# Optimization experiments

Hardware: AMD Instinct MI355X
Metric: run time of the kernel (lower is better)

## Reference

```python
import jax, jax.numpy as jnp
import numpy as np

WS = 8
HEADS = 12


def _dwconv(x, w, b):
    # x: (N, C, H, W); w: (C, 1, 3, 3) depthwise, zero pad 1
    y = jax.lax.conv_general_dilated(
        x, w, window_strides=(1, 1), padding=((1, 1), (1, 1)),
        dimension_numbers=("NCHW", "OIHW", "NCHW"), feature_group_count=x.shape[1])
    return y + b[None, :, None, None]


def _sepconv(x, dw, db, pw, pb):
    y = _dwconv(x, dw, db)
    # pointwise 1x1 conv: (N,C,H,W) x (O,C) -> (N,O,H,W)
    return jnp.einsum("nchw,oc->nohw", y, pw) + pb[None, :, None, None]


def _rel_pos_index(ws):
    coords = np.stack(np.meshgrid(np.arange(ws), np.arange(ws), indexing="ij"))  # (2, ws, ws)
    cf = coords.reshape(2, -1)
    rel = cf[:, :, None] - cf[:, None, :]          # (2, ws*ws, ws*ws)
    rel = rel.transpose(1, 2, 0).copy()
    rel[..., 0] += ws - 1
    rel[..., 1] += ws - 1
    rel[..., 0] *= 2 * ws - 1
    return rel.sum(-1)                             # (ws*ws, ws*ws)


def setup_inputs() -> dict:
    key = jax.random.key(0)
    ks = jax.random.split(key, 16)
    B, T, C, H, W = 2, 1, 384, 192, 192
    s = 0.02
    inp = {
        "vid": jax.random.normal(ks[0], (B, T, C, H, W), jnp.float32),
        "qd_w": jax.random.normal(ks[1], (C, 1, 3, 3), jnp.float32) * s,
        "qd_b": jnp.zeros((C,), jnp.float32),
        "qp_w": jax.random.normal(ks[2], (C, C), jnp.float32) * s,
        "qp_b": jnp.zeros((C,), jnp.float32),
        "kd_w": jax.random.normal(ks[3], (C, 1, 3, 3), jnp.float32) * s,
        "kd_b": jnp.zeros((C,), jnp.float32),
        "kp_w": jax.random.normal(ks[4], (C, C), jnp.float32) * s,
        "kp_b": jnp.zeros((C,), jnp.float32),
        "vd_w": jax.random.normal(ks[5], (C, 1, 3, 3), jnp.float32) * s,
        "vd_b": jnp.zeros((C,), jnp.float32),
        "vp_w": jax.random.normal(ks[6], (C, C), jnp.float32) * s,
        "vp_b": jnp.zeros((C,), jnp.float32),
        "rpb_table": jax.random.normal(ks[7], ((2 * WS - 1) ** 2, HEADS), jnp.float32) * s,
        "proj_w": jax.random.normal(ks[8], (C, C), jnp.float32) * s,
        "proj_b": jnp.zeros((C,), jnp.float32),
    }
    return inp


def reference(vid, qd_w, qd_b, qp_w, qp_b, kd_w, kd_b, kp_w, kp_b,
              vd_w, vd_b, vp_w, vp_b, rpb_table, proj_w, proj_b):
    B, T, C, H, W = vid.shape
    heads, ws = HEADS, WS
    hd = C // heads
    scale = hd ** -0.5
    x = vid.reshape(B * T, C, H, W)

    q = _sepconv(x, qd_w, qd_b, qp_w, qp_b) * scale
    k = _sepconv(x, kd_w, kd_b, kp_w, kp_b)
    v = _sepconv(x, vd_w, vd_b, vp_w, vp_b)

    nh, nw = H // ws, W // ws

    def win(z):  # (N, C, H, W) -> (N*nh*nw, heads, ws*ws, hd)
        N = z.shape[0]
        z = z.reshape(N, heads, hd, nh, ws, nw, ws)
        z = z.transpose(0, 3, 5, 1, 4, 6, 2)  # N, nh, nw, heads, ws, ws, hd
        return z.reshape(N * nh * nw, heads, ws * ws, hd)

    qw, kw, vw = win(q), win(k), win(v)

    # product search within window (dists = q . k), rel-pos bias softmax
    attn = jnp.einsum("nhqd,nhkd->nhqk", qw, kw)
    rp_idx = _rel_pos_index(ws)  # static (64, 64)
    bias = rpb_table[rp_idx.reshape(-1)].reshape(ws * ws, ws * ws, heads)
    bias = bias.transpose(2, 0, 1)  # (heads, 64, 64)
    attn = jax.nn.softmax(attn + bias[None], axis=-1)

    # weighted patch sum (ps=1 -> pixels)
    out = jnp.einsum("nhqk,nhkd->nhqd", attn, vw)  # (N*nh*nw, heads, ws*ws, hd)

    # un-window, merge heads into (h c) channel order, then token projection
    out = out.reshape(B * T, nh, nw, heads, ws, ws, hd)
    out = out.transpose(0, 1, 4, 2, 5, 3, 6).reshape(B * T, H, W, heads * hd)
    out = out @ proj_w.T + proj_b

    # fold (ps=1, stride0=1): identity overlap-add, zvid == 1
    out = out.transpose(0, 3, 1, 2).reshape(B, T, C, H, W)
    return out
```

## Files before the change

### kernel.cpp

```cpp
#include <hip/hip_runtime.h>

#define CCH 384
#define HH 192
#define WWD 192
#define NIMG 2
#define HWP (HH * WWD)
#define PTOT (NIMG * HWP)
#define HEADS 12
#define HD 32
#define NWIN 24
#define WINS 576
#define EELEM ((size_t)NIMG * CCH * HWP)
#define WMAT 147456

typedef __attribute__((ext_vector_type(8))) short bh8;
typedef __attribute__((ext_vector_type(8))) unsigned short us8;
typedef __attribute__((ext_vector_type(4))) unsigned short us4;
typedef __attribute__((ext_vector_type(4))) float fx4;

__device__ __forceinline__ unsigned short f2bf(float f) {
    unsigned u = __float_as_uint(f);
    u += 0x7fffu + ((u >> 16) & 1u);
    return (unsigned short)(u >> 16);
}

__device__ __forceinline__ void gload16(const void* g, void* l) {
    __builtin_amdgcn_global_load_lds(
        (const __attribute__((address_space(1))) void*)g,
        (__attribute__((address_space(3))) void*)l, 16, 0, 0);
}

__global__ __launch_bounds__(256) void prep(
    const float* __restrict__ qp, const float* __restrict__ kp,
    const float* __restrict__ vp, const float* __restrict__ pj,
    const float* __restrict__ qd, const float* __restrict__ kd,
    const float* __restrict__ vd, const float* __restrict__ rpb,
    unsigned short* __restrict__ Wb, float* __restrict__ dwT,
    float* __restrict__ Bx)
{
    int bx = blockIdx.x;
    if (bx < 288) {
        int idx8 = (bx * 256 + threadIdx.x) * 8;
        int which = idx8 / WMAT;
        int loc = idx8 - which * WMAT;
        const float* s = (which == 0) ? qp : (which == 1) ? kp : (which == 2) ? vp : pj;
        float4 v0 = *(const float4*)(s + loc);
        float4 v1 = *(const float4*)(s + loc + 4);
        us8 ov;
        ov[0] = f2bf(v0.x); ov[1] = f2bf(v0.y); ov[2] = f2bf(v0.z); ov[3] = f2bf(v0.w);
        ov[4] = f2bf(v1.x); ov[5] = f2bf(v1.y); ov[6] = f2bf(v1.z); ov[7] = f2bf(v1.w);
        *(us8*)(Wb + idx8) = ov;
    } else if (bx < 329) {
        int idx = (bx - 288) * 256 + threadIdx.x;
        if (idx < 3 * 9 * CCH) {
            int ten = idx / (9 * CCH);
            int rem = idx - ten * (9 * CCH);
            int tap = rem / CCH;
            int c   = rem - tap * CCH;
            const float* s = (ten == 0) ? qd : (ten == 1) ? kd : vd;
            dwT[idx] = s[c * 9 + tap];
        }
    } else {
        int idx = (bx - 329) * 256 + threadIdx.x;
        int h  = idx >> 12;
        int tk = (idx >> 6) & 63;
        int tq = idx & 63;
        int dy = (tq >> 3) - (tk >> 3) + 7;
        int dx = (tq & 7) - (tk & 7) + 7;
        Bx[idx] = rpb[(dy * 15 + dx) * HEADS + h];
    }
}

__global__ __launch_bounds__(256) void dwgather(
    const float* __restrict__ x,
    const float* __restrict__ wt,
    const float* __restrict__ qb, const float* __restrict__ kb,
    const float* __restrict__ vb,
    unsigned short* __restrict__ oq, unsigned short* __restrict__ ok,
    unsigned short* __restrict__ ov)
{
    __shared__ float halo[64 * 121];

    int bid = blockIdx.x;
    int b = (bid & 7) * 864 + (bid >> 3);
    int wtx  = b % 24;
    int strip = b / 24;
    int chv  = strip % 6;
    int nwy  = strip / 6;
    int wy   = nwy % 24;
    int n    = nwy / 24;

    int h0 = wy * 8, w0 = wtx * 8;
    int tid = threadIdx.x;
    int c   = tid & 63;
    int pxg = tid >> 6;
    int cg  = chv * 64 + c;
    int widx = n * WINS + wy * NWIN + wtx;

    const float* xbase = x + (size_t)n * CCH * HWP + (size_t)(chv * 64) * HWP;

    for (int j = tid; j < 1920; j += 256) {
        int seg = j % 3;
        int t   = j / 3;
        int rr  = t % 10;
        int cc  = t / 10;
        int hr  = h0 - 1 + rr;
        int cb  = w0 - 2 + seg * 4;
        float4 val = make_float4(0.f, 0.f, 0.f, 0.f);
        if (hr >= 0 && hr < HH) {
            const float* p = xbase + (size_t)cc * HWP + (size_t)hr * WWD;
            if (cb >= 0 && cb + 4 <= WWD) {
                val = *(const float4*)(p + cb);
            } else {
                if (cb + 0 >= 0 && cb + 0 < WWD) val.x = p[cb + 0];
                if (cb + 1 >= 0 && cb + 1 < WWD) val.y = p[cb + 1];
                if (cb + 2 >= 0 && cb + 2 < WWD) val.z = p[cb + 2];
                if (cb + 3 >= 0 && cb + 3 < WWD) val.w = p[cb + 3];
            }
        }
        int hb = cc * 121 + rr * 12 + seg * 4;
        halo[hb + 0] = val.x;
        halo[hb + 1] = val.y;
        halo[hb + 2] = val.z;
        halo[hb + 3] = val.w;
    }

    float wq[9], wk[9], wv[9];
#pragma unroll
    for (int t = 0; t < 9; ++t) {
        wq[t] = wt[t * CCH + cg];
        wk[t] = wt[9 * CCH + t * CCH + cg];
        wv[t] = wt[18 * CCH + t * CCH + cg];
    }
    float bqv = qb[cg], bkv = kb[cg], bvv = vb[cg];

    __syncthreads();

    const int hbase = c * 121 + (2 * pxg) * 12;
    float r0[10], r1[10], r2[10];
#pragma unroll
    for (int cc = 0; cc < 10; ++cc) r0[cc] = halo[hbase + cc + 1];
#pragma unroll
    for (int cc = 0; cc < 10; ++cc) r1[cc] = halo[hbase + 12 + cc + 1];
#pragma unroll
    for (int cc = 0; cc < 10; ++cc) r2[cc] = halo[hbase + 24 + cc + 1];

    size_t ob0 = ((size_t)widx * 64 + pxg * 16) * CCH + cg;

#pragma unroll
    for (int pc = 0; pc < 8; ++pc) {
        float sq = 0.f, sk = 0.f, sv = 0.f;
#pragma unroll
        for (int dc = 0; dc < 3; ++dc) {
            float x0 = r0[pc + dc], x1 = r1[pc + dc], x2 = r2[pc + dc];
            sq = fmaf(x0, wq[dc], sq);     sk = fmaf(x0, wk[dc], sk);     sv = fmaf(x0, wv[dc], sv);
            sq = fmaf(x1, wq[3 + dc], sq); sk = fmaf(x1, wk[3 + dc], sk); sv = fmaf(x1, wv[3 + dc], sv);
            sq = fmaf(x2, wq[6 + dc], sq); sk = fmaf(x2, wk[6 + dc], sk); sv = fmaf(x2, wv[6 + dc], sv);
        }
        size_t o = ob0 + (size_t)pc * CCH;
        oq[o] = f2bf(sq + bqv);
        ok[o] = f2bf(sk + bkv);
        ov[o] = f2bf(sv + bvv);
    }

#pragma unroll
    for (int cc = 0; cc < 10; ++cc) r0[cc] = halo[hbase + 36 + cc + 1];

#pragma unroll
    for (int pc = 0; pc < 8; ++pc) {
        float sq = 0.f, sk = 0.f, sv = 0.f;
#pragma unroll
        for (int dc = 0; dc < 3; ++dc) {
            float x0 = r1[pc + dc], x1 = r2[pc + dc], x2 = r0[pc + dc];
            sq = fmaf(x0, wq[dc], sq);     sk = fmaf(x0, wk[dc], sk);     sv = fmaf(x0, wv[dc], sv);
            sq = fmaf(x1, wq[3 + dc], sq); sk = fmaf(x1, wk[3 + dc], sk); sv = fmaf(x1, wv[3 + dc], sv);
            sq = fmaf(x2, wq[6 + dc], sq); sk = fmaf(x2, wk[6 + dc], sk); sv = fmaf(x2, wv[6 + dc], sv);
        }
        size_t o = ob0 + (size_t)(8 + pc) * CCH;
        oq[o] = f2bf(sq + bqv);
        ok[o] = f2bf(sk + bkv);
        ov[o] = f2bf(sv + bvv);
    }
}

__global__ __launch_bounds__(256) void qkv_gemm(
    const unsigned short* __restrict__ tr0, const unsigned short* __restrict__ tr1,
    const unsigned short* __restrict__ tr2, const unsigned short* __restrict__ Wball,
    const float* __restrict__ qpb, const float* __restrict__ kpb,
    const float* __restrict__ vpb, float scale,
    unsigned short* __restrict__ qo, unsigned short* __restrict__ ko,
    unsigned short* __restrict__ vo)
{
    __shared__ __align__(16) char smem[33792];
    typedef unsigned short (*tile3)[128][32];
    tile3 Wt = (tile3)smem;
    tile3 Yt = (tile3)(smem + 16384);
    typedef unsigned short (*tep_t)[132];
    tep_t T16 = (tep_t)smem;

    int bL = blockIdx.x;
    int O  = (bL & 7) * 648 + (bL >> 3);
    int z  = O / 1728;
    int rem = O - z * 1728;
    int py = rem / 3;
    int cx = rem - py * 3;
    int pp0 = py * 128, cm0 = cx * 128;

    const unsigned short* Y  = (z == 0) ? tr0 : (z == 1) ? tr1 : tr2;
    const unsigned short* Wb = Wball + (size_t)z * WMAT;
    const float* bias        = (z == 0) ? qpb : (z == 1) ? kpb : vpb;
    float sc                 = (z == 0) ? scale : 1.0f;
    unsigned short* outb     = (z == 0) ? qo : (z == 1) ? ko : vo;
    bool vmode = (z == 2);

    int tid = threadIdx.x;
    int lid = tid & 63, wid = tid >> 6;
    int wr = wid >> 1, wc = wid & 1;
    int li = lid & 15, g = lid >> 4;

    int srow = (lid >> 2);
    int scol = (((lid & 3) ^ ((srow >> 1) & 3))) * 8;
    int gsw = (g ^ ((li >> 1) & 3)) * 8;

    fx4 acc[4][4];
#pragma unroll
    for (int i = 0; i < 4; ++i)
#pragma unroll
        for (int j = 0; j < 4; ++j) acc[i][j] = (fx4){0.f, 0.f, 0.f, 0.f};

    tile3 A3 = vmode ? Yt : Wt;
    tile3 B3 = vmode ? Wt : Yt;

    const unsigned short* Wg0 = Wb + (size_t)(cm0 + wid * 32 + srow) * CCH + scol;
    const unsigned short* Yg0 = Y  + (size_t)(pp0 + wid * 32 + srow) * CCH + scol;

#pragma unroll
    for (int qi = 0; qi < 2; ++qi) {
        gload16(Wg0 + (size_t)qi * 16 * CCH, &Wt[0][wid * 32 + qi * 16][0]);
        gload16(Yg0 + (size_t)qi * 16 * CCH, &Yt[0][wid * 32 + qi * 16][0]);
    }
    __syncthreads();

    for (int kt = 0; kt < 12; ++kt) {
        int cur = kt & 1;
        if (kt < 11) {
            int k1 = (kt + 1) * 32;
#pragma unroll
            for (int qi = 0; qi < 2; ++qi) {
                gload16(Wg0 + (size_t)qi * 16 * CCH + k1, &Wt[cur ^ 1][wid * 32 + qi * 16][0]);
                gload16(Yg0 + (size_t)qi * 16 * CCH + k1, &Yt[cur ^ 1][wid * 32 + qi * 16][0]);
            }
        }

        bh8 a[4], b[4];
#pragma unroll
        for (int mf = 0; mf < 4; ++mf)
            a[mf] = *(const bh8*)&A3[cur][wr * 64 + mf * 16 + li][gsw];
#pragma unroll
        for (int nf = 0; nf < 4; ++nf)
            b[nf] = *(const bh8*)&B3[cur][wc * 64 + nf * 16 + li][gsw];
#pragma unroll
        for (int mf = 0; mf < 4; ++mf)
#pragma unroll
            for (int nf = 0; nf < 4; ++nf)
                acc[mf][nf] = __builtin_amdgcn_mfma_f32_16x16x32_bf16(
                    a[mf], b[nf], acc[mf][nf], 0, 0, 0);

        __syncthreads();
    }

    if (!vmode) {
#pragma unroll
        for (int mf = 0; mf < 4; ++mf) {
            int cl = wr * 64 + mf * 16 + g * 4;
            float4 bv = *(const float4*)&bias[cm0 + cl];
#pragma unroll
            for (int nf = 0; nf < 4; ++nf) {
                int pl = wc * 64 + nf * 16 + li;
                us4 o;
                o[0] = f2bf((acc[mf][nf][0] + bv.x) * sc);
                o[1] = f2bf((acc[mf][nf][1] + bv.y) * sc);
                o[2] = f2bf((acc[mf][nf][2] + bv.z) * sc);
                o[3] = f2bf((acc[mf][nf][3] + bv.w) * sc);
                *(us4*)&T16[pl][cl] = o;
            }
        }
        __syncthreads();
#pragma unroll
        for (int it = 0; it < 8; ++it) {
            int row = it * 16 + wid * 4 + (lid >> 4);
            int col = (lid & 15) * 8;
            us8 vv = *(const us8*)&T16[row][col];
            *(us8*)(outb + (size_t)(pp0 + row) * CCH + cm0 + col) = vv;
        }
    } else {
#pragma unroll
        for (int nf = 0; nf < 4; ++nf) {
            int cl = wc * 64 + nf * 16 + li;
            float bv = bias[cm0 + cl];
#pragma unroll
            for (int mf = 0; mf < 4; ++mf) {
                int pl = wr * 64 + mf * 16 + g * 4;
                us4 o;
                o[0] = f2bf(acc[mf][nf][0] + bv);
                o[1] = f2bf(acc[mf][nf][1] + bv);
                o[2] = f2bf(acc[mf][nf][2] + bv);
                o[3] = f2bf(acc[mf][nf][3] + bv);
                *(us4*)&T16[cl][pl] = o;
            }
        }
        __syncthreads();
        int n = pp0 / HWP;
        int pl0 = pp0 - n * HWP;
#pragma unroll
        for (int it = 0; it < 8; ++it) {
            int row = it * 16 + wid * 4 + (lid >> 4);
            int col = (lid & 15) * 8;
            us8 vv = *(const us8*)&T16[row][col];
            *(us8*)(outb + (size_t)(n * CCH + cm0 + row) * HWP + pl0 + col) = vv;
        }
    }
}

__global__ __launch_bounds__(256) void proj_gemm(
    const unsigned short* __restrict__ Y, const unsigned short* __restrict__ Wb,
    const float* __restrict__ bias, float* __restrict__ outf)
{
    __shared__ unsigned short Wt[2][128][32];
    __shared__ unsigned short Yt[2][128][32];

    int bL = blockIdx.x;
    int O  = (bL & 7) * 216 + (bL >> 3);
    int py = O / 3;
    int cx = O - py * 3;
    int pp0 = py * 128, cm0 = cx * 128;

    int tid = threadIdx.x;
    int lid = tid & 63, wid = tid >> 6;
    int wr = wid >> 1, wc = wid & 1;
    int li = lid & 15, g = lid >> 4;

    int srow = (lid >> 2);
    int scol = (((lid & 3) ^ ((srow >> 1) & 3))) * 8;
    int gsw = (g ^ ((li >> 1) & 3)) * 8;

    fx4 acc[4][4];
#pragma unroll
    for (int i = 0; i < 4; ++i)
#pragma unroll
        for (int j = 0; j < 4; ++j) acc[i][j] = (fx4){0.f, 0.f, 0.f, 0.f};

    const unsigned short* Wg0 = Wb + (size_t)(cm0 + wid * 32 + srow) * CCH + scol;
    const unsigned short* Yg0 = Y  + (size_t)(pp0 + wid * 32 + srow) * CCH + scol;

#pragma unroll
    for (int qi = 0; qi < 2; ++qi) {
        gload16(Wg0 + (size_t)qi * 16 * CCH, &Wt[0][wid * 32 + qi * 16][0]);
        gload16(Yg0 + (size_t)qi * 16 * CCH, &Yt[0][wid * 32 + qi * 16][0]);
    }
    __syncthreads();

    for (int kt = 0; kt < 12; ++kt) {
        int cur = kt & 1;
        if (kt < 11) {
            int k1 = (kt + 1) * 32;
#pragma unroll
            for (int qi = 0; qi < 2; ++qi) {
                gload16(Wg0 + (size_t)qi * 16 * CCH + k1, &Wt[cur ^ 1][wid * 32 + qi * 16][0]);
                gload16(Yg0 + (size_t)qi * 16 * CCH + k1, &Yt[cur ^ 1][wid * 32 + qi * 16][0]);
            }
        }

        bh8 a[4], b[4];
#pragma unroll
        for (int mf = 0; mf < 4; ++mf)
            a[mf] = *(const bh8*)&Wt[cur][wr * 64 + mf * 16 + li][gsw];
#pragma unroll
        for (int nf = 0; nf < 4; ++nf)
            b[nf] = *(const bh8*)&Yt[cur][wc * 64 + nf * 16 + li][gsw];
#pragma unroll
        for (int mf = 0; mf < 4; ++mf)
#pragma unroll
            for (int nf = 0; nf < 4; ++nf)
                acc[mf][nf] = __builtin_amdgcn_mfma_f32_16x16x32_bf16(
                    a[mf], b[nf], acc[mf][nf], 0, 0, 0);

        __syncthreads();
    }

#pragma unroll
    for (int mf = 0; mf < 4; ++mf) {
        int c = cm0 + wr * 64 + mf * 16 + g * 4;
#pragma unroll
        for (int nf = 0; nf < 4; ++nf) {
            int p = pp0 + wc * 64 + nf * 16 + li;
            int n = p / HWP;
            int rem = p - n * HWP;
            int win = rem >> 6, t = rem & 63;
            int h = (win / NWIN) * 8 + (t >> 3);
            int w = (win % NWIN) * 8 + (t & 7);
            float* op = outf + (size_t)n * CCH * HWP + (size_t)h * WWD + w;
#pragma unroll
            for (int r = 0; r < 4; ++r)
                op[(size_t)(c + r) * HWP] = acc[mf][nf][r] + bias[c + r];
        }
    }
}

__global__ __launch_bounds__(256) void attn(
    const unsigned short* __restrict__ q, const unsigned short* __restrict__ k,
    const unsigned short* __restrict__ v, const float* __restrict__ Bx,
    unsigned short* __restrict__ o)
{
    __shared__ unsigned short Pl[4][64][72];

    int tid = threadIdx.x, lid = tid & 63, wid = tid >> 6;
    int wl = blockIdx.x;
    int n = wl / WINS, winl = wl - n * WINS;
    int li = lid & 15, g = lid >> 4;

    const fx4 z = (fx4){0.f, 0.f, 0.f, 0.f};

    for (int hq = wid; hq < HEADS; hq += 4) {
        const unsigned short* qp = q + (size_t)(wl * 64) * CCH + hq * HD + g * 8;
        const unsigned short* kp = k + (size_t)(wl * 64) * CCH + hq * HD + g * 8;
        bh8 aq[4], bk[4];
#pragma unroll
        for (int mf = 0; mf < 4; ++mf)
            aq[mf] = *(const bh8*)(qp + (size_t)(mf * 16 + li) * CCH);
#pragma unroll
        for (int nf = 0; nf < 4; ++nf)
            bk[nf] = *(const bh8*)(kp + (size_t)(nf * 16 + li) * CCH);

        fx4 s[4][4];
#pragma unroll
        for (int mf = 0; mf < 4; ++mf)
#pragma unroll
            for (int nf = 0; nf < 4; ++nf)
                s[mf][nf] = __builtin_amdgcn_mfma_f32_16x16x32_bf16(aq[mf], bk[nf], z, 0, 0, 0);

#pragma unroll
        for (int mf = 0; mf < 4; ++mf)
#pragma unroll
            for (int nf = 0; nf < 4; ++nf) {
                fx4 bv = *(const fx4*)&Bx[((size_t)hq * 64 + nf * 16 + li) * 64
                                          + mf * 16 + g * 4];
                s[mf][nf] += bv;
            }

        float inv_[4][4];
#pragma unroll
        for (int mf = 0; mf < 4; ++mf)
#pragma unroll
            for (int r = 0; r < 4; ++r) {
                float m = s[mf][0][r];
#pragma unroll
                for (int nf = 1; nf < 4; ++nf) m = fmaxf(m, s[mf][nf][r]);
                m = fmaxf(m, __shfl_xor(m, 1));
                m = fmaxf(m, __shfl_xor(m, 2));
                m = fmaxf(m, __shfl_xor(m, 4));
                m = fmaxf(m, __shfl_xor(m, 8));
                float sum = 0.f;
#pragma unroll
                for (int nf = 0; nf < 4; ++nf) {
                    float e = __expf(s[mf][nf][r] - m);
                    s[mf][nf][r] = e;
                    sum += e;
                }
                sum += __shfl_xor(sum, 1);
                sum += __shfl_xor(sum, 2);
                sum += __shfl_xor(sum, 4);
                sum += __shfl_xor(sum, 8);
                inv_[mf][r] = 1.f / sum;
            }

#pragma unroll
        for (int mf = 0; mf < 4; ++mf)
#pragma unroll
            for (int nf = 0; nf < 4; ++nf)
#pragma unroll
                for (int r = 0; r < 4; ++r)
                    Pl[wid][mf * 16 + g * 4 + r][nf * 16 + li] =
                        f2bf(s[mf][nf][r] * inv_[mf][r]);

        fx4 o2[2][4];
#pragma unroll
        for (int m2 = 0; m2 < 2; ++m2)
#pragma unroll
            for (int nf = 0; nf < 4; ++nf) o2[m2][nf] = z;
#pragma unroll
        for (int ks = 0; ks < 2; ++ks) {
            bh8 av[2], bp[4];
#pragma unroll
            for (int m2 = 0; m2 < 2; ++m2)
                av[m2] = *(const bh8*)(v + (size_t)(n * CCH + hq * HD + m2 * 16 + li) * HWP
                                         + winl * 64 + ks * 32 + g * 8);
#pragma unroll
            for (int nf = 0; nf < 4; ++nf)
                bp[nf] = *(const bh8*)&Pl[wid][nf * 16 + li][ks * 32 + g * 8];
#pragma unroll
            for (int m2 = 0; m2 < 2; ++m2)
#pragma unroll
                for (int nf = 0; nf < 4; ++nf)
                    o2[m2][nf] = __builtin_amdgcn_mfma_f32_16x16x32_bf16(
                        av[m2], bp[nf], o2[m2][nf], 0, 0, 0);
        }
#pragma unroll
        for (int nf = 0; nf < 4; ++nf) {
            int tq = nf * 16 + li;
#pragma unroll
            for (int m2 = 0; m2 < 2; ++m2) {
                int d = hq * HD + m2 * 16 + g * 4;
                us4 ov;
                ov[0] = f2bf(o2[m2][nf][0]);
                ov[1] = f2bf(o2[m2][nf][1]);
                ov[2] = f2bf(o2[m2][nf][2]);
                ov[3] = f2bf(o2[m2][nf][3]);
                *(us4*)(o + (size_t)(wl * 64 + tq) * CCH + d) = ov;
            }
        }
    }
}

extern "C" void kernel_launch(void* const* d_in, const int* in_sizes, int n_in,
                              void* d_out, int out_size, void* d_ws, size_t ws_size,
                              hipStream_t stream) {
    const float* vid  = (const float*)d_in[0];
    const float* qd_w = (const float*)d_in[1];
    const float* qd_b = (const float*)d_in[2];
    const float* qp_w = (const float*)d_in[3];
    const float* qp_b = (const float*)d_in[4];
    const float* kd_w = (const float*)d_in[5];
    const float* kd_b = (const float*)d_in[6];
    const float* kp_w = (const float*)d_in[7];
    const float* kp_b = (const float*)d_in[8];
    const float* vd_w = (const float*)d_in[9];
    const float* vd_b = (const float*)d_in[10];
    const float* vp_w = (const float*)d_in[11];
    const float* vp_b = (const float*)d_in[12];
    const float* rpb  = (const float*)d_in[13];
    const float* pj_w = (const float*)d_in[14];
    const float* pj_b = (const float*)d_in[15];

    unsigned short* ws16 = (unsigned short*)d_ws;
    unsigned short* tr0 = ws16 + 3 * EELEM;
    unsigned short* tr1 = ws16 + 4 * EELEM;
    unsigned short* tr2 = ws16 + 5 * EELEM;
    unsigned short* Wb  = ws16 + 6 * EELEM;
    float* dwT          = (float*)(Wb + 4 * WMAT);
    float* Bx           = dwT + 3 * 9 * CCH;
    unsigned short* qb  = ws16;
    unsigned short* kb  = ws16 + EELEM;
    unsigned short* vb  = ws16 + 2 * EELEM;
    unsigned short* ob  = tr0;

    prep<<<521, 256, 0, stream>>>(qp_w, kp_w, vp_w, pj_w,
                                  qd_w, kd_w, vd_w, rpb, Wb, dwT, Bx);
    dwgather<<<NIMG * WINS * 6, 256, 0, stream>>>(
        vid, dwT, qd_b, kd_b, vd_b, tr0, tr1, tr2);

    const float scale = 0.17677669529663687f;
    qkv_gemm<<<5184, 256, 0, stream>>>(
        tr0, tr1, tr2, Wb, qp_b, kp_b, vp_b, scale, qb, kb, vb);

    attn<<<NIMG * WINS, 256, 0, stream>>>(qb, kb, vb, Bx, ob);

    proj_gemm<<<1728, 256, 0, stream>>>(
        ob, Wb + 3 * WMAT, pj_b, (float*)d_out);
}
```

Measured before the change: 395.2 us.

## Triple-buffer LDS tiles in QKV and projection GEMMs with one barrier per step

Both GEMM kernels move from double to triple buffering of the W and Y LDS tiles. Each k-step now uses explicit vmcnt waits and a single s_barrier, so two tiles are in flight and the trailing __syncthreads per iteration goes away. Bias values are loaded into registers before the main loop instead of in the epilogue. In exchange LDS use per block grows to 48KB, which may lower occupancy, and the vmcnt counts are hand-tuned and fragile.

```diff
diff --git a/kernel.cpp b/kernel.cpp
--- a/kernel.cpp
+++ b/kernel.cpp
@@ -183,6 +183,15 @@
     }
 }
 
+#define ISSUE_TILE(KT, BUF)                                                     \
+    do {                                                                        \
+        int k0_ = (KT) * 32;                                                    \
+        gload16(Wg0 + k0_,                     &Wt[BUF][wid * 32][0]);          \
+        gload16(Wg0 + (size_t)16 * CCH + k0_,  &Wt[BUF][wid * 32 + 16][0]);     \
+        gload16(Yg0 + k0_,                     &Yt[BUF][wid * 32][0]);          \
+        gload16(Yg0 + (size_t)16 * CCH + k0_,  &Yt[BUF][wid * 32 + 16][0]);     \
+    } while (0)
+
 __global__ __launch_bounds__(256) void qkv_gemm(
     const unsigned short* __restrict__ tr0, const unsigned short* __restrict__ tr1,
     const unsigned short* __restrict__ tr2, const unsigned short* __restrict__ Wball,
@@ -191,10 +200,10 @@
     unsigned short* __restrict__ qo, unsigned short* __restrict__ ko,
     unsigned short* __restrict__ vo)
 {
-    __shared__ __align__(16) char smem[33792];
+    __shared__ __align__(16) char smem[49152];
     typedef unsigned short (*tile3)[128][32];
     tile3 Wt = (tile3)smem;
-    tile3 Yt = (tile3)(smem + 16384);
+    tile3 Yt = (tile3)(smem + 24576);
     typedef unsigned short (*tep_t)[132];
     tep_t T16 = (tep_t)smem;
 
@@ -234,24 +243,33 @@
     const unsigned short* Wg0 = Wb + (size_t)(cm0 + wid * 32 + srow) * CCH + scol;
     const unsigned short* Yg0 = Y  + (size_t)(pp0 + wid * 32 + srow) * CCH + scol;
 
-#pragma unroll
-    for (int qi = 0; qi < 2; ++qi) {
-        gload16(Wg0 + (size_t)qi * 16 * CCH, &Wt[0][wid * 32 + qi * 16][0]);
-        gload16(Yg0 + (size_t)qi * 16 * CCH, &Yt[0][wid * 32 + qi * 16][0]);
-    }
-    __syncthreads();
-
+    float4 bv4[4];
+    float  bvs[4];
+    if (!vmode) {
+#pragma unroll
+        for (int mf = 0; mf < 4; ++mf)
+            bv4[mf] = *(const float4*)&bias[cm0 + wr * 64 + mf * 16 + g * 4];
+    } else {
+#pragma unroll
+        for (int nf = 0; nf < 4; ++nf)
+            bvs[nf] = bias[cm0 + wc * 64 + nf * 16 + li];
+    }
+    asm volatile("s_waitcnt vmcnt(0)" ::: "memory");
+    __builtin_amdgcn_sched_barrier(0);
+
+    ISSUE_TILE(0, 0);
+    ISSUE_TILE(1, 1);
+
+#pragma unroll
     for (int kt = 0; kt < 12; ++kt) {
-        int cur = kt & 1;
-        if (kt < 11) {
-            int k1 = (kt + 1) * 32;
-#pragma unroll
-            for (int qi = 0; qi < 2; ++qi) {
-                gload16(Wg0 + (size_t)qi * 16 * CCH + k1, &Wt[cur ^ 1][wid * 32 + qi * 16][0]);
-                gload16(Yg0 + (size_t)qi * 16 * CCH + k1, &Yt[cur ^ 1][wid * 32 + qi * 16][0]);
-            }
-        }
-
+        __builtin_amdgcn_sched_barrier(0);
+        if (kt < 11) asm volatile("s_waitcnt vmcnt(4)" ::: "memory");
+        else         asm volatile("s_waitcnt vmcnt(0)" ::: "memory");
+        __builtin_amdgcn_s_barrier();
+        __builtin_amdgcn_sched_barrier(0);
+        if (kt < 10) ISSUE_TILE(kt + 2, (kt + 2) % 3);
+
+        int cur = kt % 3;
         bh8 a[4], b[4];
 #pragma unroll
         for (int mf = 0; mf < 4; ++mf)
@@ -265,15 +283,15 @@
             for (int nf = 0; nf < 4; ++nf)
                 acc[mf][nf] = __builtin_amdgcn_mfma_f32_16x16x32_bf16(
                     a[mf], b[nf], acc[mf][nf], 0, 0, 0);
-
-        __syncthreads();
-    }
+    }
+
+    __syncthreads();
 
     if (!vmode) {
 #pragma unroll
         for (int mf = 0; mf < 4; ++mf) {
             int cl = wr * 64 + mf * 16 + g * 4;
-            float4 bv = *(const float4*)&bias[cm0 + cl];
+            float4 bv = bv4[mf];
 #pragma unroll
             for (int nf = 0; nf < 4; ++nf) {
                 int pl = wc * 64 + nf * 16 + li;
@@ -297,7 +315,7 @@
 #pragma unroll
         for (int nf = 0; nf < 4; ++nf) {
             int cl = wc * 64 + nf * 16 + li;
-            float bv = bias[cm0 + cl];
+            float bv = bvs[nf];
 #pragma unroll
             for (int mf = 0; mf < 4; ++mf) {
                 int pl = wr * 64 + mf * 16 + g * 4;
@@ -326,8 +344,8 @@
     const unsigned short* __restrict__ Y, const unsigned short* __restrict__ Wb,
     const float* __restrict__ bias, float* __restrict__ outf)
 {
-    __shared__ unsigned short Wt[2][128][32];
-    __shared__ unsigned short Yt[2][128][32];
+    __shared__ unsigned short Wt[3][128][32];
+    __shared__ unsigned short Yt[3][128][32];
 
     int bL = blockIdx.x;
     int O  = (bL & 7) * 216 + (bL >> 3);
@@ -353,24 +371,26 @@
     const unsigned short* Wg0 = Wb + (size_t)(cm0 + wid * 32 + srow) * CCH + scol;
     const unsigned short* Yg0 = Y  + (size_t)(pp0 + wid * 32 + srow) * CCH + scol;
 
-#pragma unroll
-    for (int qi = 0; qi < 2; ++qi) {
-        gload16(Wg0 + (size_t)qi * 16 * CCH, &Wt[0][wid * 32 + qi * 16][0]);
-        gload16(Yg0 + (size_t)qi * 16 * CCH, &Yt[0][wid * 32 + qi * 16][0]);
-    }
-    __syncthreads();
-
+    float4 bv4[4];
+#pragma unroll
+    for (int mf = 0; mf < 4; ++mf)
+        bv4[mf] = *(const float4*)&bias[cm0 + wr * 64 + mf * 16 + g * 4];
+    asm volatile("s_waitcnt vmcnt(0)" ::: "memory");
+    __builtin_amdgcn_sched_barrier(0);
+
+    ISSUE_TILE(0, 0);
+    ISSUE_TILE(1, 1);
+
+#pragma unroll
     for (int kt = 0; kt < 12; ++kt) {
-        int cur = kt & 1;
-        if (kt < 11) {
-            int k1 = (kt + 1) * 32;
-#pragma unroll
-            for (int qi = 0; qi < 2; ++qi) {
-                gload16(Wg0 + (size_t)qi * 16 * CCH + k1, &Wt[cur ^ 1][wid * 32 + qi * 16][0]);
-                gload16(Yg0 + (size_t)qi * 16 * CCH + k1, &Yt[cur ^ 1][wid * 32 + qi * 16][0]);
-            }
-        }
-
+        __builtin_amdgcn_sched_barrier(0);
+        if (kt < 11) asm volatile("s_waitcnt vmcnt(4)" ::: "memory");
+        else         asm volatile("s_waitcnt vmcnt(0)" ::: "memory");
+        __builtin_amdgcn_s_barrier();
+        __builtin_amdgcn_sched_barrier(0);
+        if (kt < 10) ISSUE_TILE(kt + 2, (kt + 2) % 3);
+
+        int cur = kt % 3;
         bh8 a[4], b[4];
 #pragma unroll
         for (int mf = 0; mf < 4; ++mf)
@@ -384,8 +404,6 @@
             for (int nf = 0; nf < 4; ++nf)
                 acc[mf][nf] = __builtin_amdgcn_mfma_f32_16x16x32_bf16(
                     a[mf], b[nf], acc[mf][nf], 0, 0, 0);
-
-        __syncthreads();
     }
 
 #pragma unroll
@@ -400,9 +418,10 @@
             int h = (win / NWIN) * 8 + (t >> 3);
             int w = (win % NWIN) * 8 + (t & 7);
             float* op = outf + (size_t)n * CCH * HWP + (size_t)h * WWD + w;
-#pragma unroll
-            for (int r = 0; r < 4; ++r)
-                op[(size_t)(c + r) * HWP] = acc[mf][nf][r] + bias[c + r];
+            op[(size_t)(c + 0) * HWP] = acc[mf][nf][0] + bv4[mf].x;
+            op[(size_t)(c + 1) * HWP] = acc[mf][nf][1] + bv4[mf].y;
+            op[(size_t)(c + 2) * HWP] = acc[mf][nf][2] + bv4[mf].z;
+            op[(size_t)(c + 3) * HWP] = acc[mf][nf][3] + bv4[mf].w;
         }
     }
 }
```

Result: faster. 373.4 us (-5.5%).
